# Performance work log

Hardware: AMD Instinct MI355X
Metric: run time of the kernel (lower is better)

## Reference

```python
import jax, jax.numpy as jnp
import numpy as np

N_RAYS = 16384
NUM_STEPS = 128
UPSAMPLE = 128
HIDDEN = 32
FEAT = 15
IMG_DIMS = 4  # latent_mode: 3 + 1
BOUND = 2.0
MIN_NEAR = 0.05


def setup_inputs() -> dict:
    key = jax.random.key(0)
    ks = jax.random.split(key, 9)
    rays_o = 0.3 * jax.random.normal(ks[0], (N_RAYS, 3), dtype=jnp.float32)
    d = jax.random.normal(ks[1], (N_RAYS, 3), dtype=jnp.float32)
    rays_d = d / jnp.linalg.norm(d, axis=-1, keepdims=True)
    W1 = 0.5 * jax.random.normal(ks[2], (3, HIDDEN), dtype=jnp.float32)
    b1 = jnp.zeros((HIDDEN,), jnp.float32)
    W2 = jax.random.normal(ks[3], (HIDDEN, 1 + FEAT), dtype=jnp.float32) / np.sqrt(HIDDEN)
    b2 = jnp.zeros((1 + FEAT,), jnp.float32)
    Wc = jax.random.normal(ks[4], (FEAT, IMG_DIMS), dtype=jnp.float32) / np.sqrt(FEAT)
    Wd = 0.5 * jax.random.normal(ks[5], (3, IMG_DIMS), dtype=jnp.float32)
    bc = jnp.zeros((IMG_DIMS,), jnp.float32)
    return {"rays_o": rays_o, "rays_d": rays_d, "W1": W1, "b1": b1,
            "W2": W2, "b2": b2, "Wc": Wc, "Wd": Wd, "bc": bc}


def _density(x, W1, b1, W2, b2):
    # x: [..., 3] -> sigma [...], feat [..., FEAT]
    h = jax.nn.relu(x @ W1 + b1)
    out = h @ W2 + b2
    return jax.nn.softplus(out[..., 0]), out[..., 1:]


def _composite_weights(z_vals, sigma, sample_dist):
    # z_vals, sigma: [N, T]; sample_dist: [N, 1]
    deltas = z_vals[..., 1:] - z_vals[..., :-1]
    deltas = jnp.concatenate(
        [deltas, jnp.broadcast_to(sample_dist, deltas[..., :1].shape)], axis=-1)
    alphas = 1.0 - jnp.exp(-deltas * sigma)
    shifted = jnp.concatenate(
        [jnp.ones_like(alphas[..., :1]), 1.0 - alphas + 1e-15], axis=-1)
    weights = alphas * jnp.cumprod(shifted, axis=-1)[..., :-1]
    return deltas, alphas, weights


def _sample_pdf(bins, weights, n_samples):
    # bins: [N, M+1], weights: [N, M] -> samples [N, n_samples] (det inverse-CDF)
    weights = weights + 1e-5
    pdf = weights / jnp.sum(weights, axis=-1, keepdims=True)
    cdf = jnp.cumsum(pdf, axis=-1)
    cdf = jnp.concatenate([jnp.zeros_like(cdf[..., :1]), cdf], axis=-1)  # [N, M+1]
    u = jnp.linspace(0.5 / n_samples, 1.0 - 0.5 / n_samples, n_samples, dtype=cdf.dtype)
    u = jnp.broadcast_to(u, (bins.shape[0], n_samples))
    inds = jax.vmap(lambda c, uu: jnp.searchsorted(c, uu, side='right'))(cdf, u)
    last = cdf.shape[-1] - 1
    below = jnp.clip(inds - 1, 0, last)
    above = jnp.clip(inds, 0, last)
    cdf_b = jnp.take_along_axis(cdf, below, axis=-1)
    cdf_a = jnp.take_along_axis(cdf, above, axis=-1)
    bins_b = jnp.take_along_axis(bins, jnp.clip(below, 0, bins.shape[-1] - 1), axis=-1)
    bins_a = jnp.take_along_axis(bins, jnp.clip(above, 0, bins.shape[-1] - 1), axis=-1)
    denom = cdf_a - cdf_b
    denom = jnp.where(denom < 1e-5, 1.0, denom)
    t = (u - cdf_b) / denom
    return bins_b + t * (bins_a - bins_b)


def reference(rays_o, rays_d, W1, b1, W2, b2, Wc, Wd, bc):
    N = rays_o.shape[0]
    # near/far from AABB [-BOUND, BOUND]^3
    inv_d = 1.0 / jnp.where(jnp.abs(rays_d) < 1e-9, 1e-9, rays_d)
    t1 = (-BOUND - rays_o) * inv_d
    t2 = (BOUND - rays_o) * inv_d
    nears = jnp.maximum(jnp.max(jnp.minimum(t1, t2), axis=-1), MIN_NEAR)[:, None]
    fars = jnp.maximum(jnp.min(jnp.maximum(t1, t2), axis=-1)[:, None], nears + 1e-5)

    # coarse stratified samples
    z = jnp.linspace(0.0, 1.0, NUM_STEPS, dtype=rays_o.dtype)[None, :]
    z_vals = nears + (fars - nears) * z  # [N, S]
    sample_dist = (fars - nears) / NUM_STEPS
    xyzs = rays_o[:, None, :] + rays_d[:, None, :] * z_vals[..., None]
    xyzs = jnp.clip(xyzs, -BOUND, BOUND)
    sigma, feat = _density(xyzs, W1, b1, W2, b2)  # [N,S], [N,S,FEAT]

    # hierarchical PDF resampling (no_grad in torch -> stop_gradient)
    deltas_c, _, w_c = _composite_weights(
        jax.lax.stop_gradient(z_vals), jax.lax.stop_gradient(sigma),
        jax.lax.stop_gradient(sample_dist))
    z_mid = jax.lax.stop_gradient(z_vals[..., :-1] + 0.5 * deltas_c[..., :-1])
    new_z = jax.lax.stop_gradient(_sample_pdf(z_mid, w_c[:, 1:-1], UPSAMPLE))
    new_xyzs = rays_o[:, None, :] + rays_d[:, None, :] * new_z[..., None]
    new_xyzs = jnp.clip(new_xyzs, -BOUND, BOUND)
    new_sigma, new_feat = _density(new_xyzs, W1, b1, W2, b2)

    # merge + sort by depth, gather everything
    z_all = jnp.concatenate([z_vals, new_z], axis=1)  # [N, S+U]
    idx = jnp.argsort(z_all, axis=1)
    z_all = jnp.take_along_axis(z_all, idx, axis=1)
    xyzs_all = jnp.take_along_axis(
        jnp.concatenate([xyzs, new_xyzs], axis=1), idx[..., None], axis=1)
    sigma_all = jnp.take_along_axis(
        jnp.concatenate([sigma, new_sigma], axis=1), idx, axis=1)
    feat_all = jnp.take_along_axis(
        jnp.concatenate([feat, new_feat], axis=1), idx[..., None], axis=1)

    # final alpha compositing
    _, alphas, weights = _composite_weights(z_all, sigma_all, sample_dist)
    dirs = jnp.broadcast_to(rays_d[:, None, :], xyzs_all.shape)
    rgbs = jax.nn.sigmoid(feat_all @ Wc + dirs @ Wd + bc)  # [N, S+U, IMG_DIMS]

    weights_sum = jnp.sum(weights, axis=-1)
    ori_z = jnp.clip((z_all - nears) / (fars - nears), 0.0, 1.0)
    depth = jnp.sum(weights * ori_z, axis=-1)
    image = jnp.sum(weights[..., None] * rgbs, axis=-2)
    image = image + (1.0 - weights_sum)[..., None] * 1.0  # bg_color = 1
    return image, depth, weights_sum
```

## Files before the change

kernel.cpp:

```cpp
#include <hip/hip_runtime.h>
#include <math.h>

#define N_RAYS 16384
#define S 128
#define FEAT 15
#define BOUNDF 2.0f
#define MIN_NEAR 0.05f
#define RPB 4
#define PRW 1152

#define O_STG  0
#define O_CDF  0
#define O_ZS   0
#define O_SIG  256
#define O_RGB  512
#define O_HU   660
#define O_HM   792
#define O_ZF   1024
#define O_AB   (PRW - 80)
#define O_BIAS (PRW - 16)

#undef O_AB
#undef O_BIAS
#undef PRW
#define PRW 1232
#define O_AB   1152
#define O_BIAS 1216

typedef __fp16 h16x2 __attribute__((ext_vector_type(2)));
typedef _Float16 f16x8 __attribute__((ext_vector_type(8)));
typedef float f32x4 __attribute__((ext_vector_type(4)));

#define WS_FRAG 0
#define WS_BF   256
#define WS_B20  260

__device__ __forceinline__ h16x2 pk_fma_f16(h16x2 a, h16x2 b, h16x2 c) {
    h16x2 d;
    asm("v_pk_fma_f16 %0, %1, %2, %3" : "=v"(d) : "v"(a), "v"(b), "v"(c));
    return d;
}
__device__ __forceinline__ h16x2 pk_relu_f16(h16x2 a) {
    h16x2 d;
    asm("v_pk_max_f16 %0, %1, 0" : "=v"(d) : "v"(a));
    return d;
}

__device__ __forceinline__ float softplus_f(float x) {
    float e = __builtin_amdgcn_exp2f(x * 1.442695041f);
    return 0.69314718056f * __builtin_amdgcn_logf(1.0f + e);
}
__device__ __forceinline__ float sigmoid_f(float x) {
    float e = __builtin_amdgcn_exp2f(x * -1.442695041f);
    return __builtin_amdgcn_rcpf(1.0f + e);
}
__device__ __forceinline__ float clampf(float x, float lo, float hi) {
    return fminf(fmaxf(x, lo), hi);
}
__device__ __forceinline__ uint2 pack_rgb(float c0, float c1, float c2, float c3) {
    h16x2 p0 = __builtin_amdgcn_cvt_pkrtz(c0, c1);
    h16x2 p1 = __builtin_amdgcn_cvt_pkrtz(c2, c3);
    uint2 r;
    r.x = __builtin_bit_cast(unsigned int, p0);
    r.y = __builtin_bit_cast(unsigned int, p1);
    return r;
}
__device__ __forceinline__ void unpack_rgb(unsigned int lo, unsigned int hi, float* c) {
    h16x2 p0 = __builtin_bit_cast(h16x2, lo);
    h16x2 p1 = __builtin_bit_cast(h16x2, hi);
    c[0] = (float)p0.x; c[1] = (float)p0.y; c[2] = (float)p1.x; c[3] = (float)p1.y;
}

template<int CTRL, int RMASK>
__device__ __forceinline__ float dppf(float old, float v) {
    int r = __builtin_amdgcn_update_dpp(__builtin_bit_cast(int, old),
                                        __builtin_bit_cast(int, v),
                                        CTRL, RMASK, 0xf, false);
    return __builtin_bit_cast(float, r);
}
template<int CTRL, int RMASK>
__device__ __forceinline__ int dppi(int old, int v) {
    return __builtin_amdgcn_update_dpp(old, v, CTRL, RMASK, 0xf, false);
}
__device__ __forceinline__ float scan_mul_f(float v) {
    v *= dppf<0x111, 0xf>(1.0f, v);
    v *= dppf<0x112, 0xf>(1.0f, v);
    v *= dppf<0x114, 0xf>(1.0f, v);
    v *= dppf<0x118, 0xf>(1.0f, v);
    v *= dppf<0x142, 0xa>(1.0f, v);
    v *= dppf<0x143, 0xc>(1.0f, v);
    return v;
}
__device__ __forceinline__ float scan_add_f(float v) {
    v += dppf<0x111, 0xf>(0.0f, v);
    v += dppf<0x112, 0xf>(0.0f, v);
    v += dppf<0x114, 0xf>(0.0f, v);
    v += dppf<0x118, 0xf>(0.0f, v);
    v += dppf<0x142, 0xa>(0.0f, v);
    v += dppf<0x143, 0xc>(0.0f, v);
    return v;
}
__device__ __forceinline__ int scan_add_i(int v) {
    v += dppi<0x111, 0xf>(0, v);
    v += dppi<0x112, 0xf>(0, v);
    v += dppi<0x114, 0xf>(0, v);
    v += dppi<0x118, 0xf>(0, v);
    v += dppi<0x142, 0xa>(0, v);
    v += dppi<0x143, 0xc>(0, v);
    return v;
}

extern "C" __global__ __launch_bounds__(64)
void nerf_prep_kernel(const float* __restrict__ W2, const float* __restrict__ b2,
                      const float* __restrict__ Wc, const float* __restrict__ bc,
                      float* __restrict__ ws) {
    const int t = threadIdx.x;
    const int col = t & 15, kb = t >> 4;
    float v[8];
#pragma unroll
    for (int j = 0; j < 8; ++j) {
        const int k = kb * 8 + j;
        float x = 0.0f;
        if (col == 0) {
            x = W2[k * 16];
        } else if (col <= 4) {
#pragma unroll
            for (int f = 0; f < FEAT; ++f) x += W2[k * 16 + 1 + f] * Wc[f * 4 + (col - 1)];
        }
        v[j] = x;
    }
#pragma unroll
    for (int m = 0; m < 4; ++m) {
        h16x2 p = __builtin_amdgcn_cvt_pkrtz(v[2 * m], v[2 * m + 1]);
        ws[WS_FRAG + t * 4 + m] = __builtin_bit_cast(float, p);
    }
    if (t < 4) {
        float b = bc[t];
#pragma unroll
        for (int f = 0; f < FEAT; ++f) b += b2[1 + f] * Wc[f * 4 + t];
        ws[WS_BF + t] = b;
    }
    if (t == 0) ws[WS_B20] = b2[0];
}

struct CoarseTag { static constexpr bool fine = false; };
struct FineTag   { static constexpr bool fine = true;  };

extern "C" __global__ __launch_bounds__(256, 6)
void nerf_render_kernel(const float* __restrict__ rays_o,
                        const float* __restrict__ rays_d,
                        const float* __restrict__ W1, const float* __restrict__ b1,
                        const float* __restrict__ Wd,
                        const float* __restrict__ wsf,
                        float* __restrict__ out) {
    const int wv   = threadIdx.x >> 6;
    const int lane = threadIdx.x & 63;
    const int ray  = blockIdx.x * RPB + wv;
    const int col16 = lane & 15;
    const int kb    = lane >> 4;

    __shared__ __align__(16) float smem[RPB][PRW];
    float*  base  = &smem[wv][0];
    float*  sStg  = base + O_STG;
    float*  sZs   = base + O_ZS;
    float*  sSig  = base + O_SIG;
    uint2*  sRgb  = (uint2*)(base + O_RGB);
    float4* sAB   = (float4*)(base + O_AB);
    float*  sBias = base + O_BIAS;
    float*  sCdf  = base + O_CDF;
    float*  sZf   = base + O_ZF;
    int*    sHU   = (int*)(base + O_HU);
    int*    sHM   = (int*)(base + O_HM);

    const float ox = rays_o[ray * 3 + 0], oy = rays_o[ray * 3 + 1], oz = rays_o[ray * 3 + 2];
    const float dx = rays_d[ray * 3 + 0], dy = rays_d[ray * 3 + 1], dz = rays_d[ray * 3 + 2];

    auto invd = [](float d) { float dd = (fabsf(d) < 1e-9f) ? 1e-9f : d; return 1.0f / dd; };
    const float ixv = invd(dx), iyv = invd(dy), izv = invd(dz);
    const float t1x = (-BOUNDF - ox) * ixv, t2x = (BOUNDF - ox) * ixv;
    const float t1y = (-BOUNDF - oy) * iyv, t2y = (BOUNDF - oy) * iyv;
    const float t1z = (-BOUNDF - oz) * izv, t2z = (BOUNDF - oz) * izv;
    float nearv = fmaxf(fmaxf(fminf(t1x, t2x), fminf(t1y, t2y)), fminf(t1z, t2z));
    nearv = fmaxf(nearv, MIN_NEAR);
    float farv = fminf(fminf(fmaxf(t1x, t2x), fmaxf(t1y, t2y)), fmaxf(t1z, t2z));
    farv = fmaxf(farv, nearv + 1e-5f);
    const float fmn = farv - nearv;
    const float sample_dist = fmn * (1.0f / (float)S);
    const float dstep = fmn * (1.0f / 127.0f);

    sHU[lane] = 0; sHU[64 + lane] = 0;
    sHM[lane] = 0; sHM[64 + lane] = 0;
    if (lane == 0) { sHU[128] = 0; sHM[128] = 0; }

    if (lane < 32) {
        const int j = lane;
        const float w0 = W1[j], w1 = W1[32 + j], w2 = W1[64 + j];
        ((float*)&sAB[j >> 1])[(j & 1)]     = b1[j] + ox * w0 + oy * w1 + oz * w2;
        ((float*)&sAB[j >> 1])[2 + (j & 1)] = dx * w0 + dy * w1 + dz * w2;
    }
    if (lane < 16) {
        float b = 0.0f;
        if (lane == 0) b = wsf[WS_B20];
        else if (lane <= 4) {
            const int c = lane - 1;
            b = wsf[WS_BF + c] + dx * Wd[c] + dy * Wd[4 + c] + dz * Wd[8 + c];
        }
        sBias[lane] = b;
    }
    __builtin_amdgcn_wave_barrier();

    h16x2 Af[4], Bf[4];
#pragma unroll
    for (int m = 0; m < 4; ++m) {
        const float4 ab = sAB[kb * 4 + m];
        Af[m] = __builtin_amdgcn_cvt_pkrtz(ab.x, ab.y);
        Bf[m] = __builtin_amdgcn_cvt_pkrtz(ab.z, ab.w);
    }
    const float4 frw = ((const float4*)wsf)[lane];
    const f16x8 bfrag = __builtin_bit_cast(f16x8, frw);
    const float bv = sBias[col16];
    f32x4 accB; accB[0] = bv; accB[1] = bv; accB[2] = bv; accB[3] = bv;

    auto mfma_pass = [&](auto tag) {
#pragma unroll
        for (int t = 0; t < 8; ++t) {
            float zs;
            if constexpr (decltype(tag)::fine) zs = sZf[t * 16 + col16];
            else                               zs = fmaf((float)(t * 16 + col16), dstep, nearv);
            const h16x2 z2 = __builtin_amdgcn_cvt_pkrtz(zs, zs);
            h16x2 h0 = pk_relu_f16(pk_fma_f16(Bf[0], z2, Af[0]));
            h16x2 h1 = pk_relu_f16(pk_fma_f16(Bf[1], z2, Af[1]));
            h16x2 h2 = pk_relu_f16(pk_fma_f16(Bf[2], z2, Af[2]));
            h16x2 h3 = pk_relu_f16(pk_fma_f16(Bf[3], z2, Af[3]));
            uint4 au;
            au.x = __builtin_bit_cast(unsigned int, h0);
            au.y = __builtin_bit_cast(unsigned int, h1);
            au.z = __builtin_bit_cast(unsigned int, h2);
            au.w = __builtin_bit_cast(unsigned int, h3);
            const f16x8 afrag = __builtin_bit_cast(f16x8, au);
            f32x4 acc = __builtin_amdgcn_mfma_f32_16x16x32_f16(afrag, bfrag, accB, 0, 0, 0);
            if (col16 < 5) {
#pragma unroll
                for (int i = 0; i < 4; ++i)
                    sStg[col16 * 132 + t * 16 + kb * 4 + i] = acc[i];
            }
        }
    };
    auto readback = [&](int p, float& sg, uint2& rgb) {
        const float c0 = sStg[0 * 132 + p];
        const float c1 = sStg[1 * 132 + p];
        const float c2 = sStg[2 * 132 + p];
        const float c3 = sStg[3 * 132 + p];
        const float c4 = sStg[4 * 132 + p];
        sg  = softplus_f(c0);
        rgb = pack_rgb(sigmoid_f(c1), sigmoid_f(c2), sigmoid_f(c3), sigmoid_f(c4));
    };

    mfma_pass(CoarseTag{});
    __builtin_amdgcn_wave_barrier();
    float sgc0, sgc1; uint2 rc0, rc1;
    readback(2 * lane,     sgc0, rc0);
    readback(2 * lane + 1, sgc1, rc1);
    const float zc0 = fmaf((float)(2 * lane), dstep, nearv);
    const float zc1 = zc0 + dstep;
    __builtin_amdgcn_wave_barrier();

    const float dc1 = (lane == 63) ? sample_dist : dstep;
    const float ec0 = __builtin_amdgcn_exp2f(dstep * sgc0 * -1.442695041f);
    const float ec1 = __builtin_amdgcn_exp2f(dc1 * sgc1 * -1.442695041f);
    const float alc0 = 1.f - ec0, alc1 = 1.f - ec1;
    const float vc0 = ec0 + 1e-15f, vc1 = ec1 + 1e-15f;
    const float incl = scan_mul_f(vc0 * vc1);
    float excl = __shfl_up(incl, 1, 64);
    if (lane == 0) excl = 1.f;
    const float wc0 = alc0 * excl;
    const float wc1 = alc1 * (excl * vc0);

    const float wnext = __shfl_down(wc0, 1, 64);
    float p0 = wc1 + 1e-5f, p1 = wnext + 1e-5f;
    if (lane == 63) { p0 = 0.f; p1 = 0.f; }
    const float s01 = p0 + p1;
    const float cinc = scan_add_f(s01);
    const float total = __builtin_bit_cast(float,
        __builtin_amdgcn_readlane(__builtin_bit_cast(int, cinc), 63));
    const float rtot = __builtin_amdgcn_rcpf(total);
    const float cexcl = cinc - s01;
    if (lane < 63) {
        const float cdfA = (cexcl + p0) * rtot;
        const float cdfB = (cexcl + p0 + p1) * rtot;
        sCdf[2 * lane + 1] = cdfA;
        sCdf[2 * lane + 2] = cdfB;
        int cA = (int)ceilf(fmaf(128.f, cdfA, -0.5f));
        int cB = (int)ceilf(fmaf(128.f, cdfB, -0.5f));
        cA = min(max(cA, 0), 128); cB = min(max(cB, 0), 128);
        atomicAdd(&sHU[cA], 1);
        atomicAdd(&sHU[cB], 1);
    } else {
        sCdf[0] = 0.f;
        atomicAdd(&sHU[0], 1);
    }
    __builtin_amdgcn_wave_barrier();

    const int2 hu = *(const int2*)(sHU + 2 * lane);
    const int hs = hu.x + hu.y;
    const int hscan = scan_add_i(hs);
    const int hexcl = hscan - hs;
    const int indsA = hexcl + hu.x;
    const int indsB = hexcl + hs;

    auto lerp_z = [&](int inds, float u) -> float {
        const int below = inds - 1;
        const int above = min(inds, 126);
        const float cb = sCdf[below], ca = sCdf[above];
        const float bb = fmaf((float)below + 0.5f, dstep, nearv);
        const float ba = fmaf((float)above + 0.5f, dstep, nearv);
        float den = ca - cb;
        if (den < 1e-5f) den = 1.0f;
        const float t = (u - cb) * __builtin_amdgcn_rcpf(den);
        return bb + t * (ba - bb);
    };
    const float zf0 = lerp_z(indsA, ((float)(2 * lane) + 0.5f) * (1.0f / 128.f));
    const float zf1 = lerp_z(indsB, ((float)(2 * lane) + 1.5f) * (1.0f / 128.f));
    sZf[2 * lane]     = zf0;
    sZf[2 * lane + 1] = zf1;

    const float inv_stepz = 127.0f / fmn;
    int r0 = (int)floorf((zf0 - nearv) * inv_stepz) + 1;
    int r1 = (int)floorf((zf1 - nearv) * inv_stepz) + 1;
    r0 = min(max(r0, 0), 128); r1 = min(max(r1, 0), 128);
    atomicAdd(&sHM[r0], 1);
    atomicAdd(&sHM[r1], 1);
    __builtin_amdgcn_wave_barrier();

    mfma_pass(FineTag{});
    __builtin_amdgcn_wave_barrier();
    float sgf0, sgf1; uint2 rf0, rf1;
    readback(2 * lane,     sgf0, rf0);
    readback(2 * lane + 1, sgf1, rf1);
    __builtin_amdgcn_wave_barrier();

    const int2 hm = *(const int2*)(sHM + 2 * lane);
    const int ms = hm.x + hm.y;
    const int mscan = scan_add_i(ms);
    const int mexcl = mscan - ms;
    const int dC0 = 2 * lane + (mexcl + hm.x);
    const int dC1 = 2 * lane + 1 + (mexcl + ms);
    const int dF0 = 2 * lane + r0;
    const int dF1 = 2 * lane + 1 + r1;

    auto il = [](int d) { return ((d & 3) << 6) + (d >> 2); };
    {
        const int a0 = il(dC0), a1 = il(dC1), a2 = il(dF0), a3 = il(dF1);
        sZs[a0] = zc0; sSig[a0] = sgc0; sRgb[a0] = rc0;
        sZs[a1] = zc1; sSig[a1] = sgc1; sRgb[a1] = rc1;
        sZs[a2] = zf0; sSig[a2] = sgf0; sRgb[a2] = rf0;
        sZs[a3] = zf1; sSig[a3] = sgf1; sRgb[a3] = rf1;
    }
    __builtin_amdgcn_wave_barrier();

    const float z0 = sZs[lane],        z1 = sZs[64 + lane];
    const float z2 = sZs[128 + lane],  z3 = sZs[192 + lane];
    const float g0 = sSig[lane],       g1 = sSig[64 + lane];
    const float g2 = sSig[128 + lane], g3 = sSig[192 + lane];
    const uint2 q0 = sRgb[lane],       q1 = sRgb[64 + lane];
    const uint2 q2 = sRgb[128 + lane], q3 = sRgb[192 + lane];

    const float znx = __shfl_down(z0, 1, 64);
    const float dd0 = z1 - z0;
    const float dd1 = z2 - z1;
    const float dd2 = z3 - z2;
    const float dd3 = (lane == 63) ? sample_dist : (znx - z3);

    const float e0 = __builtin_amdgcn_exp2f(dd0 * g0 * -1.442695041f);
    const float e1 = __builtin_amdgcn_exp2f(dd1 * g1 * -1.442695041f);
    const float e2 = __builtin_amdgcn_exp2f(dd2 * g2 * -1.442695041f);
    const float e3 = __builtin_amdgcn_exp2f(dd3 * g3 * -1.442695041f);
    const float al0 = 1.f - e0, al1 = 1.f - e1, al2 = 1.f - e2, al3 = 1.f - e3;
    const float v0 = e0 + 1e-15f, v1 = e1 + 1e-15f, v2 = e2 + 1e-15f, v3 = e3 + 1e-15f;

    const float incl2 = scan_mul_f(v0 * v1 * v2 * v3);
    float T0 = __shfl_up(incl2, 1, 64);
    if (lane == 0) T0 = 1.f;
    const float T1 = T0 * v0, T2 = T1 * v1, T3 = T2 * v2;
    const float w0 = al0 * T0, w1 = al1 * T1, w2 = al2 * T2, w3 = al3 * T3;

    const float inv_fn = 1.0f / fmn;
    const float oz0 = clampf((z0 - nearv) * inv_fn, 0.f, 1.f);
    const float oz1 = clampf((z1 - nearv) * inv_fn, 0.f, 1.f);
    const float oz2 = clampf((z2 - nearv) * inv_fn, 0.f, 1.f);
    const float oz3 = clampf((z3 - nearv) * inv_fn, 0.f, 1.f);

    float r0c[4], r1c[4], r2c[4], r3c[4];
    unpack_rgb(q0.x, q0.y, r0c);
    unpack_rgb(q1.x, q1.y, r1c);
    unpack_rgb(q2.x, q2.y, r2c);
    unpack_rgb(q3.x, q3.y, r3c);

    float vals[6];
#pragma unroll
    for (int c = 0; c < 4; ++c)
        vals[c] = w0 * r0c[c] + w1 * r1c[c] + w2 * r2c[c] + w3 * r3c[c];
    vals[4] = w0 * oz0 + w1 * oz1 + w2 * oz2 + w3 * oz3;
    vals[5] = w0 + w1 + w2 + w3;

#pragma unroll
    for (int q = 0; q < 6; ++q) vals[q] = scan_add_f(vals[q]);

    if (lane == 63) {
        const float wsum = vals[5];
#pragma unroll
        for (int c = 0; c < 4; ++c)
            out[ray * 4 + c] = vals[c] + (1.0f - wsum);
        out[4 * N_RAYS + ray] = vals[4];
        out[5 * N_RAYS + ray] = wsum;
    }
}

extern "C" void kernel_launch(void* const* d_in, const int* in_sizes, int n_in,
                              void* d_out, int out_size, void* d_ws, size_t ws_size,
                              hipStream_t stream) {
    const float* rays_o = (const float*)d_in[0];
    const float* rays_d = (const float*)d_in[1];
    const float* W1 = (const float*)d_in[2];
    const float* b1 = (const float*)d_in[3];
    const float* W2 = (const float*)d_in[4];
    const float* b2 = (const float*)d_in[5];
    const float* Wc = (const float*)d_in[6];
    const float* Wd = (const float*)d_in[7];
    const float* bc = (const float*)d_in[8];
    float* out = (float*)d_out;
    float* ws  = (float*)d_ws;

    hipLaunchKernelGGL(nerf_prep_kernel, dim3(1), dim3(64), 0, stream,
                       W2, b2, Wc, bc, ws);
    hipLaunchKernelGGL(nerf_render_kernel, dim3(N_RAYS / RPB), dim3(256), 0, stream,
                       rays_o, rays_d, W1, b1, Wd, ws, out);
}
```

Before: 33.64 us.

## Pack two rays per wavefront with 32-lane segmented scans

Each 64-lane wavefront now handles two rays, one per 32-lane half, with 4 samples per lane in the coarse and fine stages and 8 in compositing. Scans drop the cross-half DPP step so they run segmented, and shared-memory accesses become vectorized. Blocks shrink to 128 threads while still covering 4 rays. The MFMA pass still runs over 16-wide tiles, so each wave issues both rays' MFMA passes, trading more serial work per wave for fewer waves and less per-ray scan and barrier overhead.

New measurement: 34.31 us. 1.02x slower.

```diff
diff --git a/kernel.cpp b/kernel.cpp
--- a/kernel.cpp
+++ b/kernel.cpp
@@ -2,12 +2,11 @@
 #include <math.h>
 
 #define N_RAYS 16384
-#define S 128
 #define FEAT 15
 #define BOUNDF 2.0f
 #define MIN_NEAR 0.05f
+#define PRW 1232
 #define RPB 4
-#define PRW 1152
 
 #define O_STG  0
 #define O_CDF  0
@@ -17,19 +16,13 @@
 #define O_HU   660
 #define O_HM   792
 #define O_ZF   1024
-#define O_AB   (PRW - 80)
-#define O_BIAS (PRW - 16)
-
-#undef O_AB
-#undef O_BIAS
-#undef PRW
-#define PRW 1232
 #define O_AB   1152
 #define O_BIAS 1216
 
 typedef __fp16 h16x2 __attribute__((ext_vector_type(2)));
 typedef _Float16 f16x8 __attribute__((ext_vector_type(8)));
 typedef float f32x4 __attribute__((ext_vector_type(4)));
+typedef float f32x2v __attribute__((ext_vector_type(2)));
 
 #define WS_FRAG 0
 #define WS_BF   256
@@ -45,7 +38,6 @@
     asm("v_pk_max_f16 %0, %1, 0" : "=v"(d) : "v"(a));
     return d;
 }
-
 __device__ __forceinline__ float softplus_f(float x) {
     float e = __builtin_amdgcn_exp2f(x * 1.442695041f);
     return 0.69314718056f * __builtin_amdgcn_logf(1.0f + e);
@@ -82,31 +74,28 @@
 __device__ __forceinline__ int dppi(int old, int v) {
     return __builtin_amdgcn_update_dpp(old, v, CTRL, RMASK, 0xf, false);
 }
-__device__ __forceinline__ float scan_mul_f(float v) {
+__device__ __forceinline__ float seg_scan_mul(float v) {
     v *= dppf<0x111, 0xf>(1.0f, v);
     v *= dppf<0x112, 0xf>(1.0f, v);
     v *= dppf<0x114, 0xf>(1.0f, v);
     v *= dppf<0x118, 0xf>(1.0f, v);
     v *= dppf<0x142, 0xa>(1.0f, v);
-    v *= dppf<0x143, 0xc>(1.0f, v);
     return v;
 }
-__device__ __forceinline__ float scan_add_f(float v) {
+__device__ __forceinline__ float seg_scan_add(float v) {
     v += dppf<0x111, 0xf>(0.0f, v);
     v += dppf<0x112, 0xf>(0.0f, v);
     v += dppf<0x114, 0xf>(0.0f, v);
     v += dppf<0x118, 0xf>(0.0f, v);
     v += dppf<0x142, 0xa>(0.0f, v);
-    v += dppf<0x143, 0xc>(0.0f, v);
     return v;
 }
-__device__ __forceinline__ int scan_add_i(int v) {
+__device__ __forceinline__ int seg_scan_add_i(int v) {
     v += dppi<0x111, 0xf>(0, v);
     v += dppi<0x112, 0xf>(0, v);
     v += dppi<0x114, 0xf>(0, v);
     v += dppi<0x118, 0xf>(0, v);
     v += dppi<0x142, 0xa>(0, v);
-    v += dppi<0x143, 0xc>(0, v);
     return v;
 }
 
@@ -143,34 +132,27 @@
     if (t == 0) ws[WS_B20] = b2[0];
 }
 
-struct CoarseTag { static constexpr bool fine = false; };
-struct FineTag   { static constexpr bool fine = true;  };
-
-extern "C" __global__ __launch_bounds__(256, 6)
+extern "C" __global__ __launch_bounds__(128, 4)
 void nerf_render_kernel(const float* __restrict__ rays_o,
                         const float* __restrict__ rays_d,
                         const float* __restrict__ W1, const float* __restrict__ b1,
                         const float* __restrict__ Wd,
                         const float* __restrict__ wsf,
                         float* __restrict__ out) {
-    const int wv   = threadIdx.x >> 6;
-    const int lane = threadIdx.x & 63;
-    const int ray  = blockIdx.x * RPB + wv;
+    const int wv    = threadIdx.x >> 6;
+    const int lane  = threadIdx.x & 63;
+    const int seg   = lane >> 5;
+    const int sl    = lane & 31;
     const int col16 = lane & 15;
     const int kb    = lane >> 4;
+    const int ray   = blockIdx.x * RPB + wv * 2 + seg;
 
     __shared__ __align__(16) float smem[RPB][PRW];
-    float*  base  = &smem[wv][0];
-    float*  sStg  = base + O_STG;
-    float*  sZs   = base + O_ZS;
-    float*  sSig  = base + O_SIG;
-    uint2*  sRgb  = (uint2*)(base + O_RGB);
-    float4* sAB   = (float4*)(base + O_AB);
-    float*  sBias = base + O_BIAS;
-    float*  sCdf  = base + O_CDF;
-    float*  sZf   = base + O_ZF;
-    int*    sHU   = (int*)(base + O_HU);
-    int*    sHM   = (int*)(base + O_HM);
+    float* baseO = &smem[wv * 2 + seg][0];
+    float* base0 = &smem[wv * 2 + 0][0];
+    float* base1 = &smem[wv * 2 + 1][0];
+    int*   sHUo  = (int*)(baseO + O_HU);
+    int*   sHMo  = (int*)(baseO + O_HM);
 
     const float ox = rays_o[ray * 3 + 0], oy = rays_o[ray * 3 + 1], oz = rays_o[ray * 3 + 2];
     const float dx = rays_d[ray * 3 + 0], dy = rays_d[ray * 3 + 1], dz = rays_d[ray * 3 + 2];
@@ -185,48 +167,61 @@
     float farv = fminf(fminf(fmaxf(t1x, t2x), fmaxf(t1y, t2y)), fmaxf(t1z, t2z));
     farv = fmaxf(farv, nearv + 1e-5f);
     const float fmn = farv - nearv;
-    const float sample_dist = fmn * (1.0f / (float)S);
+    const float sample_dist = fmn * (1.0f / 128.0f);
     const float dstep = fmn * (1.0f / 127.0f);
 
-    sHU[lane] = 0; sHU[64 + lane] = 0;
-    sHM[lane] = 0; sHM[64 + lane] = 0;
-    if (lane == 0) { sHU[128] = 0; sHM[128] = 0; }
-
-    if (lane < 32) {
-        const int j = lane;
+    {
+        int4 z4i; z4i.x = 0; z4i.y = 0; z4i.z = 0; z4i.w = 0;
+        *(int4*)(sHUo + 4 * sl) = z4i;
+        *(int4*)(sHMo + 4 * sl) = z4i;
+        if (sl == 0) { sHUo[128] = 0; sHMo[128] = 0; }
+    }
+
+    {
+        const int j = sl;
         const float w0 = W1[j], w1 = W1[32 + j], w2 = W1[64 + j];
-        ((float*)&sAB[j >> 1])[(j & 1)]     = b1[j] + ox * w0 + oy * w1 + oz * w2;
-        ((float*)&sAB[j >> 1])[2 + (j & 1)] = dx * w0 + dy * w1 + dz * w2;
-    }
-    if (lane < 16) {
+        float* sABo = baseO + O_AB;
+        sABo[(j >> 1) * 4 + (j & 1)]     = b1[j] + ox * w0 + oy * w1 + oz * w2;
+        sABo[(j >> 1) * 4 + 2 + (j & 1)] = dx * w0 + dy * w1 + dz * w2;
+    }
+    if (sl < 16) {
         float b = 0.0f;
-        if (lane == 0) b = wsf[WS_B20];
-        else if (lane <= 4) {
-            const int c = lane - 1;
+        if (sl == 0) b = wsf[WS_B20];
+        else if (sl <= 4) {
+            const int c = sl - 1;
             b = wsf[WS_BF + c] + dx * Wd[c] + dy * Wd[4 + c] + dz * Wd[8 + c];
         }
-        sBias[lane] = b;
-    }
-    __builtin_amdgcn_wave_barrier();
-
-    h16x2 Af[4], Bf[4];
+        (baseO + O_BIAS)[sl] = b;
+    }
+    __builtin_amdgcn_wave_barrier();
+
+    const float nv0 = __shfl(nearv, 0, 64),  nv1 = __shfl(nearv, 32, 64);
+    const float dt0 = __shfl(dstep, 0, 64),  dt1 = __shfl(dstep, 32, 64);
+
+    h16x2 Af0[4], Bf0[4], Af1[4], Bf1[4];
 #pragma unroll
     for (int m = 0; m < 4; ++m) {
-        const float4 ab = sAB[kb * 4 + m];
-        Af[m] = __builtin_amdgcn_cvt_pkrtz(ab.x, ab.y);
-        Bf[m] = __builtin_amdgcn_cvt_pkrtz(ab.z, ab.w);
+        const float4 a0 = ((const float4*)(base0 + O_AB))[kb * 4 + m];
+        Af0[m] = __builtin_amdgcn_cvt_pkrtz(a0.x, a0.y);
+        Bf0[m] = __builtin_amdgcn_cvt_pkrtz(a0.z, a0.w);
+        const float4 a1 = ((const float4*)(base1 + O_AB))[kb * 4 + m];
+        Af1[m] = __builtin_amdgcn_cvt_pkrtz(a1.x, a1.y);
+        Bf1[m] = __builtin_amdgcn_cvt_pkrtz(a1.z, a1.w);
     }
     const float4 frw = ((const float4*)wsf)[lane];
     const f16x8 bfrag = __builtin_bit_cast(f16x8, frw);
-    const float bv = sBias[col16];
-    f32x4 accB; accB[0] = bv; accB[1] = bv; accB[2] = bv; accB[3] = bv;
-
-    auto mfma_pass = [&](auto tag) {
-#pragma unroll
-        for (int t = 0; t < 8; ++t) {
+    const float bv0 = (base0 + O_BIAS)[col16];
+    const float bv1 = (base1 + O_BIAS)[col16];
+    f32x4 acc0; acc0[0] = bv0; acc0[1] = bv0; acc0[2] = bv0; acc0[3] = bv0;
+    f32x4 acc1; acc1[0] = bv1; acc1[1] = bv1; acc1[2] = bv1; acc1[3] = bv1;
+
+    auto mlp_pass = [&](float* stg, const float* zsrc, float nv, float dt,
+                        const h16x2* Af, const h16x2* Bf, const f32x4& accB) {
+#pragma unroll
+        for (int tt = 0; tt < 8; ++tt) {
             float zs;
-            if constexpr (decltype(tag)::fine) zs = sZf[t * 16 + col16];
-            else                               zs = fmaf((float)(t * 16 + col16), dstep, nearv);
+            if (zsrc) zs = zsrc[tt * 16 + col16];
+            else      zs = fmaf((float)(tt * 16 + col16), dt, nv);
             const h16x2 z2 = __builtin_amdgcn_cvt_pkrtz(zs, zs);
             h16x2 h0 = pk_relu_f16(pk_fma_f16(Bf[0], z2, Af[0]));
             h16x2 h1 = pk_relu_f16(pk_fma_f16(Bf[1], z2, Af[1]));
@@ -239,79 +234,91 @@
             au.w = __builtin_bit_cast(unsigned int, h3);
             const f16x8 afrag = __builtin_bit_cast(f16x8, au);
             f32x4 acc = __builtin_amdgcn_mfma_f32_16x16x32_f16(afrag, bfrag, accB, 0, 0, 0);
-            if (col16 < 5) {
-#pragma unroll
-                for (int i = 0; i < 4; ++i)
-                    sStg[col16 * 132 + t * 16 + kb * 4 + i] = acc[i];
+            if (col16 < 5)
+                *(f32x4*)&stg[col16 * 132 + tt * 16 + kb * 4] = acc;
+        }
+    };
+    auto readback = [&](float* sg, uint2* rgb) {
+        const f32x4 c0 = *(const f32x4*)&baseO[O_STG + 0 * 132 + 4 * sl];
+        const f32x4 c1 = *(const f32x4*)&baseO[O_STG + 1 * 132 + 4 * sl];
+        const f32x4 c2 = *(const f32x4*)&baseO[O_STG + 2 * 132 + 4 * sl];
+        const f32x4 c3 = *(const f32x4*)&baseO[O_STG + 3 * 132 + 4 * sl];
+        const f32x4 c4 = *(const f32x4*)&baseO[O_STG + 4 * 132 + 4 * sl];
+#pragma unroll
+        for (int i = 0; i < 4; ++i) {
+            sg[i]  = softplus_f(c0[i]);
+            rgb[i] = pack_rgb(sigmoid_f(c1[i]), sigmoid_f(c2[i]),
+                              sigmoid_f(c3[i]), sigmoid_f(c4[i]));
+        }
+    };
+
+    mlp_pass(base0 + O_STG, nullptr, nv0, dt0, Af0, Bf0, acc0);
+    mlp_pass(base1 + O_STG, nullptr, nv1, dt1, Af1, Bf1, acc1);
+    __builtin_amdgcn_wave_barrier();
+    float sgc[4]; uint2 rgc[4];
+    readback(sgc, rgc);
+    __builtin_amdgcn_wave_barrier();
+
+    float alc[4], vvc[4];
+#pragma unroll
+    for (int c = 0; c < 4; ++c) {
+        float del = (sl == 31 && c == 3) ? sample_dist : dstep;
+        const float e = __builtin_amdgcn_exp2f(del * sgc[c] * -1.442695041f);
+        alc[c] = 1.0f - e;
+        vvc[c] = e + 1e-15f;
+    }
+    const float incl = seg_scan_mul(vvc[0] * vvc[1] * vvc[2] * vvc[3]);
+    float excl = __shfl_up(incl, 1, 64);
+    if (sl == 0) excl = 1.0f;
+    const float w0c = alc[0] * excl;
+    const float w1c = alc[1] * excl * vvc[0];
+    const float w2c = alc[2] * excl * vvc[0] * vvc[1];
+    const float w3c = alc[3] * excl * vvc[0] * vvc[1] * vvc[2];
+
+    const float wnext = __shfl_down(w0c, 1, 64);
+    float p0 = w1c + 1e-5f, p1 = w2c + 1e-5f, p2 = w3c + 1e-5f, p3 = wnext + 1e-5f;
+    if (sl == 31) { p2 = 0.0f; p3 = 0.0f; }
+    const float psum = p0 + p1 + p2 + p3;
+    const float cinc = seg_scan_add(psum);
+    const float total = __shfl(cinc, (lane & 32) | 31, 64);
+    const float rtot = __builtin_amdgcn_rcpf(total);
+    const float cexcl = cinc - psum;
+    {
+        float cs = cexcl;
+        const float pv[4] = {p0, p1, p2, p3};
+#pragma unroll
+        for (int c = 0; c < 4; ++c) {
+            cs += pv[c];
+            const int idx = 4 * sl + 1 + c;
+            if (idx <= 126) {
+                const float val = cs * rtot;
+                baseO[O_CDF + idx] = val;
+                int cnt = (int)ceilf(fmaf(128.0f, val, -0.5f));
+                cnt = min(max(cnt, 0), 128);
+                atomicAdd(&sHUo[cnt], 1);
             }
         }
-    };
-    auto readback = [&](int p, float& sg, uint2& rgb) {
-        const float c0 = sStg[0 * 132 + p];
-        const float c1 = sStg[1 * 132 + p];
-        const float c2 = sStg[2 * 132 + p];
-        const float c3 = sStg[3 * 132 + p];
-        const float c4 = sStg[4 * 132 + p];
-        sg  = softplus_f(c0);
-        rgb = pack_rgb(sigmoid_f(c1), sigmoid_f(c2), sigmoid_f(c3), sigmoid_f(c4));
-    };
-
-    mfma_pass(CoarseTag{});
-    __builtin_amdgcn_wave_barrier();
-    float sgc0, sgc1; uint2 rc0, rc1;
-    readback(2 * lane,     sgc0, rc0);
-    readback(2 * lane + 1, sgc1, rc1);
-    const float zc0 = fmaf((float)(2 * lane), dstep, nearv);
-    const float zc1 = zc0 + dstep;
-    __builtin_amdgcn_wave_barrier();
-
-    const float dc1 = (lane == 63) ? sample_dist : dstep;
-    const float ec0 = __builtin_amdgcn_exp2f(dstep * sgc0 * -1.442695041f);
-    const float ec1 = __builtin_amdgcn_exp2f(dc1 * sgc1 * -1.442695041f);
-    const float alc0 = 1.f - ec0, alc1 = 1.f - ec1;
-    const float vc0 = ec0 + 1e-15f, vc1 = ec1 + 1e-15f;
-    const float incl = scan_mul_f(vc0 * vc1);
-    float excl = __shfl_up(incl, 1, 64);
-    if (lane == 0) excl = 1.f;
-    const float wc0 = alc0 * excl;
-    const float wc1 = alc1 * (excl * vc0);
-
-    const float wnext = __shfl_down(wc0, 1, 64);
-    float p0 = wc1 + 1e-5f, p1 = wnext + 1e-5f;
-    if (lane == 63) { p0 = 0.f; p1 = 0.f; }
-    const float s01 = p0 + p1;
-    const float cinc = scan_add_f(s01);
-    const float total = __builtin_bit_cast(float,
-        __builtin_amdgcn_readlane(__builtin_bit_cast(int, cinc), 63));
-    const float rtot = __builtin_amdgcn_rcpf(total);
-    const float cexcl = cinc - s01;
-    if (lane < 63) {
-        const float cdfA = (cexcl + p0) * rtot;
-        const float cdfB = (cexcl + p0 + p1) * rtot;
-        sCdf[2 * lane + 1] = cdfA;
-        sCdf[2 * lane + 2] = cdfB;
-        int cA = (int)ceilf(fmaf(128.f, cdfA, -0.5f));
-        int cB = (int)ceilf(fmaf(128.f, cdfB, -0.5f));
-        cA = min(max(cA, 0), 128); cB = min(max(cB, 0), 128);
-        atomicAdd(&sHU[cA], 1);
-        atomicAdd(&sHU[cB], 1);
-    } else {
-        sCdf[0] = 0.f;
-        atomicAdd(&sHU[0], 1);
-    }
-    __builtin_amdgcn_wave_barrier();
-
-    const int2 hu = *(const int2*)(sHU + 2 * lane);
-    const int hs = hu.x + hu.y;
-    const int hscan = scan_add_i(hs);
+        if (sl == 31) {
+            baseO[O_CDF + 0] = 0.0f;
+            atomicAdd(&sHUo[0], 1);
+        }
+    }
+    __builtin_amdgcn_wave_barrier();
+
+    const int4 hu = *(const int4*)(sHUo + 4 * sl);
+    const int hs = hu.x + hu.y + hu.z + hu.w;
+    const int hscan = seg_scan_add_i(hs);
     const int hexcl = hscan - hs;
-    const int indsA = hexcl + hu.x;
-    const int indsB = hexcl + hs;
-
-    auto lerp_z = [&](int inds, float u) -> float {
-        const int below = inds - 1;
-        const int above = min(inds, 126);
-        const float cb = sCdf[below], ca = sCdf[above];
+    int inds[4];
+    inds[0] = hexcl + hu.x;
+    inds[1] = inds[0] + hu.y;
+    inds[2] = inds[1] + hu.z;
+    inds[3] = inds[2] + hu.w;
+
+    auto lerp_z = [&](int ii, float u) -> float {
+        const int below = ii - 1;
+        const int above = min(ii, 126);
+        const float cb = baseO[O_CDF + below], ca = baseO[O_CDF + above];
         const float bb = fmaf((float)below + 0.5f, dstep, nearv);
         const float ba = fmaf((float)above + 0.5f, dstep, nearv);
         float den = ca - cb;
@@ -319,94 +326,102 @@
         const float t = (u - cb) * __builtin_amdgcn_rcpf(den);
         return bb + t * (ba - bb);
     };
-    const float zf0 = lerp_z(indsA, ((float)(2 * lane) + 0.5f) * (1.0f / 128.f));
-    const float zf1 = lerp_z(indsB, ((float)(2 * lane) + 1.5f) * (1.0f / 128.f));
-    sZf[2 * lane]     = zf0;
-    sZf[2 * lane + 1] = zf1;
-
+    float zff[4]; int rr[4];
     const float inv_stepz = 127.0f / fmn;
-    int r0 = (int)floorf((zf0 - nearv) * inv_stepz) + 1;
-    int r1 = (int)floorf((zf1 - nearv) * inv_stepz) + 1;
-    r0 = min(max(r0, 0), 128); r1 = min(max(r1, 0), 128);
-    atomicAdd(&sHM[r0], 1);
-    atomicAdd(&sHM[r1], 1);
-    __builtin_amdgcn_wave_barrier();
-
-    mfma_pass(FineTag{});
-    __builtin_amdgcn_wave_barrier();
-    float sgf0, sgf1; uint2 rf0, rf1;
-    readback(2 * lane,     sgf0, rf0);
-    readback(2 * lane + 1, sgf1, rf1);
-    __builtin_amdgcn_wave_barrier();
-
-    const int2 hm = *(const int2*)(sHM + 2 * lane);
-    const int ms = hm.x + hm.y;
-    const int mscan = scan_add_i(ms);
+#pragma unroll
+    for (int c = 0; c < 4; ++c) {
+        const float u = ((float)(4 * sl + c) + 0.5f) * (1.0f / 128.0f);
+        zff[c] = lerp_z(inds[c], u);
+        int r = (int)floorf((zff[c] - nearv) * inv_stepz) + 1;
+        rr[c] = min(max(r, 0), 128);
+        atomicAdd(&sHMo[rr[c]], 1);
+    }
+    {
+        f32x4 zfv; zfv[0] = zff[0]; zfv[1] = zff[1]; zfv[2] = zff[2]; zfv[3] = zff[3];
+        *(f32x4*)&baseO[O_ZF + 4 * sl] = zfv;
+    }
+    __builtin_amdgcn_wave_barrier();
+
+    mlp_pass(base0 + O_STG, base0 + O_ZF, nv0, dt0, Af0, Bf0, acc0);
+    mlp_pass(base1 + O_STG, base1 + O_ZF, nv1, dt1, Af1, Bf1, acc1);
+    __builtin_amdgcn_wave_barrier();
+    float sgf[4]; uint2 rgf[4];
+    readback(sgf, rgf);
+    __builtin_amdgcn_wave_barrier();
+
+    const int4 hm = *(const int4*)(sHMo + 4 * sl);
+    const int ms = hm.x + hm.y + hm.z + hm.w;
+    const int mscan = seg_scan_add_i(ms);
     const int mexcl = mscan - ms;
-    const int dC0 = 2 * lane + (mexcl + hm.x);
-    const int dC1 = 2 * lane + 1 + (mexcl + ms);
-    const int dF0 = 2 * lane + r0;
-    const int dF1 = 2 * lane + 1 + r1;
+    int gpre[4];
+    gpre[0] = mexcl + hm.x;
+    gpre[1] = gpre[0] + hm.y;
+    gpre[2] = gpre[1] + hm.z;
+    gpre[3] = gpre[2] + hm.w;
 
     auto il = [](int d) { return ((d & 3) << 6) + (d >> 2); };
-    {
-        const int a0 = il(dC0), a1 = il(dC1), a2 = il(dF0), a3 = il(dF1);
-        sZs[a0] = zc0; sSig[a0] = sgc0; sRgb[a0] = rc0;
-        sZs[a1] = zc1; sSig[a1] = sgc1; sRgb[a1] = rc1;
-        sZs[a2] = zf0; sSig[a2] = sgf0; sRgb[a2] = rf0;
-        sZs[a3] = zf1; sSig[a3] = sgf1; sRgb[a3] = rf1;
-    }
-    __builtin_amdgcn_wave_barrier();
-
-    const float z0 = sZs[lane],        z1 = sZs[64 + lane];
-    const float z2 = sZs[128 + lane],  z3 = sZs[192 + lane];
-    const float g0 = sSig[lane],       g1 = sSig[64 + lane];
-    const float g2 = sSig[128 + lane], g3 = sSig[192 + lane];
-    const uint2 q0 = sRgb[lane],       q1 = sRgb[64 + lane];
-    const uint2 q2 = sRgb[128 + lane], q3 = sRgb[192 + lane];
-
-    const float znx = __shfl_down(z0, 1, 64);
-    const float dd0 = z1 - z0;
-    const float dd1 = z2 - z1;
-    const float dd2 = z3 - z2;
-    const float dd3 = (lane == 63) ? sample_dist : (znx - z3);
-
-    const float e0 = __builtin_amdgcn_exp2f(dd0 * g0 * -1.442695041f);
-    const float e1 = __builtin_amdgcn_exp2f(dd1 * g1 * -1.442695041f);
-    const float e2 = __builtin_amdgcn_exp2f(dd2 * g2 * -1.442695041f);
-    const float e3 = __builtin_amdgcn_exp2f(dd3 * g3 * -1.442695041f);
-    const float al0 = 1.f - e0, al1 = 1.f - e1, al2 = 1.f - e2, al3 = 1.f - e3;
-    const float v0 = e0 + 1e-15f, v1 = e1 + 1e-15f, v2 = e2 + 1e-15f, v3 = e3 + 1e-15f;
-
-    const float incl2 = scan_mul_f(v0 * v1 * v2 * v3);
-    float T0 = __shfl_up(incl2, 1, 64);
-    if (lane == 0) T0 = 1.f;
-    const float T1 = T0 * v0, T2 = T1 * v1, T3 = T2 * v2;
-    const float w0 = al0 * T0, w1 = al1 * T1, w2 = al2 * T2, w3 = al3 * T3;
+    uint2* sRgbO = (uint2*)(baseO + O_RGB);
+#pragma unroll
+    for (int c = 0; c < 4; ++c) {
+        const int idx = 4 * sl + c;
+        const float zc = fmaf((float)idx, dstep, nearv);
+        const int aC = il(idx + gpre[c]);
+        baseO[O_ZS + aC] = zc;  baseO[O_SIG + aC] = sgc[c];  sRgbO[aC] = rgc[c];
+        const int aF = il(idx + rr[c]);
+        baseO[O_ZS + aF] = zff[c]; baseO[O_SIG + aF] = sgf[c]; sRgbO[aF] = rgf[c];
+    }
+    __builtin_amdgcn_wave_barrier();
+
+    float z_[8], g_[8]; uint2 q_[8];
+#pragma unroll
+    for (int row = 0; row < 4; ++row) {
+        const f32x2v zz = *(const f32x2v*)&baseO[O_ZS + row * 64 + 2 * sl];
+        const f32x2v gg = *(const f32x2v*)&baseO[O_SIG + row * 64 + 2 * sl];
+        const uint4  qq = *(const uint4*)(sRgbO + row * 64 + 2 * sl);
+        z_[row] = zz[0]; z_[row + 4] = zz[1];
+        g_[row] = gg[0]; g_[row + 4] = gg[1];
+        q_[row].x = qq.x; q_[row].y = qq.y;
+        q_[row + 4].x = qq.z; q_[row + 4].y = qq.w;
+    }
+
+    float dd[8];
+#pragma unroll
+    for (int c = 0; c < 7; ++c) dd[c] = z_[c + 1] - z_[c];
+    const float znext = __shfl_down(z_[0], 1, 64);
+    dd[7] = (sl == 31) ? sample_dist : (znext - z_[7]);
+
+    float al[8], v[8];
+#pragma unroll
+    for (int c = 0; c < 8; ++c) {
+        const float e = __builtin_amdgcn_exp2f(dd[c] * g_[c] * -1.442695041f);
+        al[c] = 1.0f - e;
+        v[c] = e + 1e-15f;
+    }
+    float prod = v[0];
+#pragma unroll
+    for (int c = 1; c < 8; ++c) prod *= v[c];
+    const float incl2 = seg_scan_mul(prod);
+    float T = __shfl_up(incl2, 1, 64);
+    if (sl == 0) T = 1.0f;
 
     const float inv_fn = 1.0f / fmn;
-    const float oz0 = clampf((z0 - nearv) * inv_fn, 0.f, 1.f);
-    const float oz1 = clampf((z1 - nearv) * inv_fn, 0.f, 1.f);
-    const float oz2 = clampf((z2 - nearv) * inv_fn, 0.f, 1.f);
-    const float oz3 = clampf((z3 - nearv) * inv_fn, 0.f, 1.f);
-
-    float r0c[4], r1c[4], r2c[4], r3c[4];
-    unpack_rgb(q0.x, q0.y, r0c);
-    unpack_rgb(q1.x, q1.y, r1c);
-    unpack_rgb(q2.x, q2.y, r2c);
-    unpack_rgb(q3.x, q3.y, r3c);
-
-    float vals[6];
-#pragma unroll
-    for (int c = 0; c < 4; ++c)
-        vals[c] = w0 * r0c[c] + w1 * r1c[c] + w2 * r2c[c] + w3 * r3c[c];
-    vals[4] = w0 * oz0 + w1 * oz1 + w2 * oz2 + w3 * oz3;
-    vals[5] = w0 + w1 + w2 + w3;
-
-#pragma unroll
-    for (int q = 0; q < 6; ++q) vals[q] = scan_add_f(vals[q]);
-
-    if (lane == 63) {
+    float vals[6] = {0.f, 0.f, 0.f, 0.f, 0.f, 0.f};
+#pragma unroll
+    for (int c = 0; c < 8; ++c) {
+        const float w = al[c] * T;
+        float rc[4];
+        unpack_rgb(q_[c].x, q_[c].y, rc);
+        vals[0] += w * rc[0]; vals[1] += w * rc[1];
+        vals[2] += w * rc[2]; vals[3] += w * rc[3];
+        const float ozv = clampf((z_[c] - nearv) * inv_fn, 0.0f, 1.0f);
+        vals[4] += w * ozv;
+        vals[5] += w;
+        T *= v[c];
+    }
+#pragma unroll
+    for (int q = 0; q < 6; ++q) vals[q] = seg_scan_add(vals[q]);
+
+    if (sl == 31) {
         const float wsum = vals[5];
 #pragma unroll
         for (int c = 0; c < 4; ++c)
@@ -433,6 +448,6 @@
 
     hipLaunchKernelGGL(nerf_prep_kernel, dim3(1), dim3(64), 0, stream,
                        W2, b2, Wc, bc, ws);
-    hipLaunchKernelGGL(nerf_render_kernel, dim3(N_RAYS / RPB), dim3(256), 0, stream,
+    hipLaunchKernelGGL(nerf_render_kernel, dim3(N_RAYS / RPB), dim3(128), 0, stream,
                        rays_o, rays_d, W1, b1, Wd, ws, out);
 }
```
